# Kernel tuning notes

Measured on AMD Instinct MI355X. Metric: run time of the kernel, lower is better.

Reference implementation:

```python
import jax, jax.numpy as jnp
import numpy as np
from jax import lax

B = 128      # graphs per batch
N = 68       # facial landmarks (num_nodes per graph)
C = 3        # input channels
P = 32       # PATCH_SIZE
K = 16       # NUM_KERNELS
FD = 64      # feature_dim
GH = 128     # gcn_hidden_dim
OUT = 2      # output_dim
EG = 8 * N   # edges per graph
T = B * N    # total nodes


def setup_inputs() -> dict:
    key = jax.random.key(0)
    ks = jax.random.split(key, 8)
    x = jax.random.normal(ks[0], (T, C, P, P), jnp.float32)
    e = jax.random.randint(ks[1], (2, B, EG), 0, N)
    offs = (jnp.arange(B) * N)[None, :, None]
    edge_index = (e + offs).reshape(2, -1)            # within-graph edges, global ids
    batch = jnp.repeat(jnp.arange(B), N)              # node -> graph id
    conv_w = jax.random.normal(ks[2], (N, K, C, 3, 3), jnp.float32) * 0.05
    conv_b = jnp.zeros((N, K), jnp.float32)
    lin1_w = jax.random.normal(ks[3], (N, K * (P // 2) * (P // 2), FD), jnp.float32) * 0.02
    lin1_b = jnp.zeros((N, FD), jnp.float32)
    gcn_w = jax.random.normal(ks[4], (FD, GH), jnp.float32) * 0.1
    gcn_b = jnp.zeros((GH,), jnp.float32)
    mlp_w1 = jax.random.normal(ks[5], (GH, GH // 2), jnp.float32) * 0.1
    mlp_b1 = jnp.zeros((GH // 2,), jnp.float32)
    mlp_w2 = jax.random.normal(ks[6], (GH // 2, OUT), jnp.float32) * 0.1
    mlp_b2 = jnp.zeros((OUT,), jnp.float32)
    return dict(x=x, edge_index=edge_index, batch=batch, conv_w=conv_w, conv_b=conv_b,
                lin1_w=lin1_w, lin1_b=lin1_b, gcn_w=gcn_w, gcn_b=gcn_b,
                mlp_w1=mlp_w1, mlp_b1=mlp_b1, mlp_w2=mlp_w2, mlp_b2=mlp_b2)


def reference(x, edge_index, batch, conv_w, conv_b, lin1_w, lin1_b,
              gcn_w, gcn_b, mlp_w1, mlp_b1, mlp_w2, mlp_b2):
    # --- per-node-type CNN routing (nodes are laid out [graph, local_index]) ---
    xr = x.reshape(B, N, C, P, P)

    def cnn_one(xn, w, b):           # xn: [B,C,P,P]  w: [K,C,3,3]
        y = lax.conv_general_dilated(xn, w, (1, 1), 'SAME',
                                     dimension_numbers=('NCHW', 'OIHW', 'NCHW'))
        return jax.nn.relu(y + b[None, :, None, None])

    a = jax.vmap(cnn_one, in_axes=(1, 0, 0), out_axes=1)(xr, conv_w, conv_b)  # [B,N,K,P,P]
    pooled = lax.reduce_window(a, -jnp.inf, lax.max,
                               (1, 1, 1, 2, 2), (1, 1, 1, 2, 2), 'VALID')     # [B,N,K,P/2,P/2]
    flat = pooled.reshape(B, N, -1)
    feats = jax.nn.relu(jnp.einsum('bnf,nfo->bno', flat, lin1_w) + lin1_b[None])  # [B,N,FD]
    nodes = feats.reshape(T, FD)

    # --- GCNConv: add self-loops, symmetric normalization ---
    loop = jnp.arange(T)
    src = jnp.concatenate([edge_index[0], loop])
    dst = jnp.concatenate([edge_index[1], loop])
    deg = jax.ops.segment_sum(jnp.ones_like(dst, jnp.float32), dst, T)
    dis = jnp.where(deg > 0, 1.0 / jnp.sqrt(deg), 0.0)
    norm = dis[src] * dis[dst]
    xw = nodes @ gcn_w                                   # [T,GH]
    h = jax.ops.segment_sum(norm[:, None] * xw[src], dst, T) + gcn_b
    h = jax.nn.relu(h)

    # --- global mean pool over graphs ---
    cnt = jax.ops.segment_sum(jnp.ones((T,), jnp.float32), batch, B)
    g = jax.ops.segment_sum(h, batch, B) / cnt[:, None]  # [B,GH]

    # --- MLP head ---
    z = jax.nn.relu(g @ mlp_w1 + mlp_b1)
    return z @ mlp_w2 + mlp_b2                           # [B,OUT]
```

## Files before the change

### kernel.cpp

```cpp
#include <hip/hip_runtime.h>
#include <hip/hip_fp16.h>

#define B_   128
#define N_   68
#define C_   3
#define P_   32
#define K_   16
#define FD_  64
#define GH_  128
#define EG_  544
#define T_   8704
#define FLAT_ 4096
#define FCH_ 16

typedef __attribute__((ext_vector_type(8))) _Float16 half8;
typedef __attribute__((ext_vector_type(2))) _Float16 half2v;
typedef __attribute__((ext_vector_type(4))) float   floatx4;

__global__ __launch_bounds__(256) void conv_pool_kernel(
    const float* __restrict__ x, const float* __restrict__ conv_w,
    const float* __restrict__ conv_b, _Float16* __restrict__ pooled) {
  const int t = blockIdx.x;
  const int n = t % N_;
  const int tid = threadIdx.x;

  __shared__ float xs[3 * 34 * 34];
  __shared__ float wS[K_ * 28];

  {
    const float* wp = conv_w + (size_t)n * (K_ * 27);
    const float* bp = conv_b + (size_t)n * K_;
    for (int i = tid; i < K_ * 28; i += 256) {
      int k = i / 28, j = i - k * 28;
      wS[i] = (j < 27) ? wp[k * 27 + j] : bp[k];
    }
  }
  for (int i = tid; i < 396; i += 256) {
    int c = i / 132, j = i - c * 132;
    int off;
    if (j < 34)       off = j;
    else if (j < 68)  off = 33 * 34 + (j - 34);
    else if (j < 100) off = (j - 68 + 1) * 34;
    else              off = (j - 100 + 1) * 34 + 33;
    xs[c * 1156 + off] = 0.0f;
  }
  const float4* xg = (const float4*)(x + (size_t)t * (C_ * P_ * P_));
  #pragma unroll
  for (int j = 0; j < 3; j++) {
    int i4 = tid + j * 256;
    float4 v = xg[i4];
    int f0 = i4 * 4;
    int c = f0 >> 10, rem = f0 & 1023, y = rem >> 5, xc = rem & 31;
    float* dstp = &xs[c * 1156 + (y + 1) * 34 + xc + 1];
    dstp[0] = v.x; dstp[1] = v.y; dstp[2] = v.z; dstp[3] = v.w;
  }
  __syncthreads();

  const int py = tid >> 4, px = tid & 15;

  float xr[3][4][4];
  #pragma unroll
  for (int c = 0; c < 3; c++)
    #pragma unroll
    for (int r = 0; r < 4; r++)
      #pragma unroll
      for (int cc = 0; cc < 4; cc++)
        xr[c][r][cc] = xs[c * 1156 + (2 * py + r) * 34 + (2 * px + cc)];

  _Float16* outp = pooled + (size_t)t * FLAT_ + py * 16 + px;

  #pragma unroll 2
  for (int k = 0; k < K_; k++) {
    float w[28];
    const float4* wk4 = (const float4*)&wS[k * 28];
    #pragma unroll
    for (int q4 = 0; q4 < 7; q4++) *(float4*)&w[q4 * 4] = wk4[q4];
    float bk = w[27];
    float a00 = bk, a01 = bk, a10 = bk, a11 = bk;
    #pragma unroll
    for (int c = 0; c < 3; c++)
      #pragma unroll
      for (int dy = 0; dy < 3; dy++)
        #pragma unroll
        for (int dx = 0; dx < 3; dx++) {
          float wv = w[c * 9 + dy * 3 + dx];
          a00 += xr[c][dy][dx]         * wv;
          a01 += xr[c][dy][dx + 1]     * wv;
          a10 += xr[c][dy + 1][dx]     * wv;
          a11 += xr[c][dy + 1][dx + 1] * wv;
        }
    float m = fmaxf(fmaxf(a00, a01), fmaxf(a10, a11));
    m = fmaxf(m, 0.0f);
    outp[k * 256] = (_Float16)m;
  }
}

__global__ __launch_bounds__(256) void lin1_mfma_kernel(
    const _Float16* __restrict__ pooled, const float* __restrict__ lin1_w,
    float* __restrict__ part) {
  const int n   = blockIdx.x >> 4;
  const int fc  = blockIdx.x & 15;
  const int tid = threadIdx.x;
  const int wave = tid >> 6, lane = tid & 63;
  const int q = lane >> 4, lr = lane & 15;

  __shared__ __align__(16) _Float16 As[128 * 72];
  __shared__ __align__(16) _Float16 Bt[64 * 72];

  floatx4 acc[2][4];
  #pragma unroll
  for (int mt = 0; mt < 2; mt++)
    #pragma unroll
    for (int nt = 0; nt < 4; nt++)
      acc[mt][nt] = (floatx4){0.f, 0.f, 0.f, 0.f};

  const int f_base = fc * 256;
  for (int step = 0; step < 4; step++) {
    const int f0 = f_base + step * 64;

    #pragma unroll
    for (int j = 0; j < 4; j++) {
      int idx = tid + j * 256;
      int r = idx >> 3, ch = idx & 7;
      uint4 v = *(const uint4*)&pooled[(size_t)(r * N_ + n) * FLAT_ + f0 + ch * 8];
      *(uint4*)&As[r * 72 + ch * 8] = v;
    }
    const float* wg = &lin1_w[(size_t)n * (FLAT_ * FD_) + (size_t)f0 * FD_];
    #pragma unroll
    for (int it = 0; it < 2; it++) {
      int p = tid + it * 256;
      int o0 = (p & 15) * 4, k0 = (p >> 4) * 2;
      const float* wgk = wg + k0 * 64 + o0;
      float4 va = *(const float4*)wgk;
      float4 vb = *(const float4*)(wgk + 64);
      *(half2v*)&Bt[(o0 + 0) * 72 + k0] = (half2v){(_Float16)va.x, (_Float16)vb.x};
      *(half2v*)&Bt[(o0 + 1) * 72 + k0] = (half2v){(_Float16)va.y, (_Float16)vb.y};
      *(half2v*)&Bt[(o0 + 2) * 72 + k0] = (half2v){(_Float16)va.z, (_Float16)vb.z};
      *(half2v*)&Bt[(o0 + 3) * 72 + k0] = (half2v){(_Float16)va.w, (_Float16)vb.w};
    }
    __syncthreads();

    #pragma unroll
    for (int kh = 0; kh < 2; kh++) {
      half8 af[2], bf[4];
      #pragma unroll
      for (int mt = 0; mt < 2; mt++)
        af[mt] = *(const half8*)&As[(wave * 32 + mt * 16 + lr) * 72 + kh * 32 + q * 8];
      #pragma unroll
      for (int nt = 0; nt < 4; nt++)
        bf[nt] = *(const half8*)&Bt[(nt * 16 + lr) * 72 + kh * 32 + q * 8];
      #pragma unroll
      for (int mt = 0; mt < 2; mt++)
        #pragma unroll
        for (int nt = 0; nt < 4; nt++)
          acc[mt][nt] = __builtin_amdgcn_mfma_f32_16x16x32_f16(
              af[mt], bf[nt], acc[mt][nt], 0, 0, 0);
    }
    __syncthreads();
  }

  float* pb = part + (size_t)fc * T_ * FD_;
  #pragma unroll
  for (int mt = 0; mt < 2; mt++) {
    #pragma unroll
    for (int v = 0; v < 4; v++) {
      int r = wave * 32 + mt * 16 + q * 4 + v;
      size_t base = (size_t)(r * N_ + n) * FD_;
      #pragma unroll
      for (int nt = 0; nt < 4; nt++)
        pb[base + nt * 16 + lr] = acc[mt][nt][v];
    }
  }
}

__global__ __launch_bounds__(256) void feats_kernel(
    const float* __restrict__ part, const float* __restrict__ lin1_b,
    float* __restrict__ feats) {
  int gid = blockIdx.x * 256 + threadIdx.x;
  int t = gid >> 4, f4 = (gid & 15) * 4;
  int n = t % N_;
  float4 s = *(const float4*)&lin1_b[n * FD_ + f4];
  #pragma unroll
  for (int fc = 0; fc < FCH_; fc++) {
    float4 v = *(const float4*)&part[((size_t)fc * T_ + t) * FD_ + f4];
    s.x += v.x; s.y += v.y; s.z += v.z; s.w += v.w;
  }
  s.x = fmaxf(s.x, 0.f); s.y = fmaxf(s.y, 0.f);
  s.z = fmaxf(s.z, 0.f); s.w = fmaxf(s.w, 0.f);
  *(float4*)&feats[(size_t)t * FD_ + f4] = s;
}

__global__ __launch_bounds__(256) void gcn_agg_kernel(
    const float* __restrict__ feats, const int* __restrict__ edge_index,
    float* __restrict__ agg) {
  const int b  = blockIdx.x >> 1;
  const int fh = blockIdx.x & 1;
  const int tid = threadIdx.x;

  __shared__ float fS[N_ * 33], aS[N_ * 33];
  __shared__ int   esrcS[EG_], edstS[EG_];
  __shared__ float nrmS[EG_];
  __shared__ int   degS[N_];
  __shared__ float disS[N_];

  if (tid < N_) degS[tid] = 0;
  const int* srcp = edge_index;
  const int* dstp = edge_index + (B_ * EG_);
  const int e0 = b * EG_, nbase = b * N_;
  for (int e = tid; e < EG_; e += 256) {
    esrcS[e] = srcp[e0 + e] - nbase;
    edstS[e] = dstp[e0 + e] - nbase;
  }
  for (int idx = tid; idx < N_ * 32; idx += 256) {
    int i = idx >> 5, f = idx & 31;
    fS[i * 33 + f] = feats[(size_t)(b * N_ + i) * FD_ + fh * 32 + f];
  }
  __syncthreads();
  for (int e = tid; e < EG_; e += 256) atomicAdd(&degS[edstS[e]], 1);
  __syncthreads();
  if (tid < N_) disS[tid] = rsqrtf((float)(degS[tid] + 1));
  __syncthreads();
  for (int e = tid; e < EG_; e += 256)
    nrmS[e] = disS[esrcS[e]] * disS[edstS[e]];
  for (int idx = tid; idx < N_ * 32; idx += 256) {
    int i = idx >> 5, f = idx & 31;
    float d = disS[i];
    aS[i * 33 + f] = d * d * fS[i * 33 + f];
  }
  __syncthreads();
  for (int idx = tid; idx < EG_ * 32; idx += 256) {
    int e = idx >> 5, f = idx & 31;
    atomicAdd(&aS[edstS[e] * 33 + f], nrmS[e] * fS[esrcS[e] * 33 + f]);
  }
  __syncthreads();
  for (int idx = tid; idx < N_ * 32; idx += 256) {
    int i = idx >> 5, f = idx & 31;
    agg[(size_t)(b * N_ + i) * FD_ + fh * 32 + f] = aS[i * 33 + f];
  }
}

__global__ __launch_bounds__(512) void gcn_head_kernel(
    const float* __restrict__ agg, const float* __restrict__ gcn_w,
    const float* __restrict__ gcn_b, const float* __restrict__ w1,
    const float* __restrict__ b1, const float* __restrict__ w2,
    const float* __restrict__ b2, float* __restrict__ out) {
  const int b = blockIdx.x;
  const int tid = threadIdx.x;

  __shared__ float aS[N_ * 68];
  __shared__ float wS[FD_ * GH_];
  __shared__ float gP[4][GH_];
  __shared__ float z1S[64];

  for (int i4 = tid; i4 < N_ * 16; i4 += 512) {
    int i = i4 >> 4, qf = (i4 & 15) * 4;
    *(float4*)&aS[i * 68 + qf] = *(const float4*)&agg[(size_t)(b * N_ + i) * FD_ + qf];
  }
  #pragma unroll
  for (int j = 0; j < 4; j++)
    ((float4*)wS)[tid + j * 512] = ((const float4*)gcn_w)[tid + j * 512];
  __syncthreads();

  const int j = tid & 127, ig = tid >> 7;
  float wc[64];
  #pragma unroll
  for (int k = 0; k < 64; k++) wc[k] = wS[k * GH_ + j];
  const float bias = gcn_b[j];
  float gsum = 0.f;
  for (int i = ig; i < N_; i += 4) {
    float acc = bias;
    #pragma unroll
    for (int kq = 0; kq < 16; kq++) {
      float4 a = *(const float4*)&aS[i * 68 + kq * 4];
      acc += a.x * wc[kq * 4] + a.y * wc[kq * 4 + 1]
           + a.z * wc[kq * 4 + 2] + a.w * wc[kq * 4 + 3];
    }
    gsum += fmaxf(acc, 0.f);
  }
  gP[ig][j] = gsum;
  __syncthreads();
  if (tid < GH_)
    gP[0][tid] = (gP[0][tid] + gP[1][tid] + gP[2][tid] + gP[3][tid]) * (1.f / 68.f);
  __syncthreads();
  if (tid < 64) {
    float s = b1[tid];
    #pragma unroll 8
    for (int jj = 0; jj < GH_; jj++) s += gP[0][jj] * w1[jj * 64 + tid];
    z1S[tid] = fmaxf(s, 0.f);
  }
  __syncthreads();
  if (tid < 2) {
    float s = b2[tid];
    #pragma unroll 8
    for (int jj = 0; jj < 64; jj++) s += z1S[jj] * w2[jj * 2 + tid];
    out[b * 2 + tid] = s;
  }
}

extern "C" void kernel_launch(void* const* d_in, const int* in_sizes, int n_in,
                              void* d_out, int out_size, void* d_ws, size_t ws_size,
                              hipStream_t stream) {
  const float* x        = (const float*)d_in[0];
  const int*   edge_idx = (const int*)d_in[1];
  const float* conv_w   = (const float*)d_in[3];
  const float* conv_b   = (const float*)d_in[4];
  const float* lin1_w   = (const float*)d_in[5];
  const float* lin1_b   = (const float*)d_in[6];
  const float* gcn_w    = (const float*)d_in[7];
  const float* gcn_b    = (const float*)d_in[8];
  const float* mlp_w1   = (const float*)d_in[9];
  const float* mlp_b1   = (const float*)d_in[10];
  const float* mlp_w2   = (const float*)d_in[11];
  const float* mlp_b2   = (const float*)d_in[12];
  float* outp = (float*)d_out;

  char* wsb = (char*)d_ws;
  _Float16* pooled = (_Float16*)wsb;
  float* part  = (float*)(wsb + (size_t)T_ * FLAT_ * 2);
  float* feats = part + (size_t)FCH_ * T_ * FD_;
  float* agg   = feats + (size_t)T_ * FD_;

  conv_pool_kernel<<<T_, 256, 0, stream>>>(x, conv_w, conv_b, pooled);
  lin1_mfma_kernel<<<N_ * FCH_, 256, 0, stream>>>(pooled, lin1_w, part);
  feats_kernel<<<544, 256, 0, stream>>>(part, lin1_b, feats);
  gcn_agg_kernel<<<B_ * 2, 256, 0, stream>>>(feats, edge_idx, agg);
  gcn_head_kernel<<<B_, 512, 0, stream>>>(agg, gcn_w, gcn_b,
                                          mlp_w1, mlp_b1, mlp_w2, mlp_b2, outp);
}
```

Baseline: 355.7 us.

## Fuse GCN tail kernels, prefetch lin1 tiles, pack conv FMAs into float2

Merges feats reduction, GCN aggregation and head into one kernel per graph, which removes two launches and the feats/agg round trips through global memory. lin1 now prefetches the next A/B tile into registers while the MFMAs on the current tile run. The conv kernel packs row pairs into float2 vectors so the compiler can emit packed FMAs, and it adds an occupancy hint to its launch bounds. The fused tail uses fewer blocks (128 instead of 256 for aggregation) and more LDS per block, so parallelism in that stage drops.

```diff
diff --git a/kernel.cpp b/kernel.cpp
--- a/kernel.cpp
+++ b/kernel.cpp
@@ -16,8 +16,9 @@
 typedef __attribute__((ext_vector_type(8))) _Float16 half8;
 typedef __attribute__((ext_vector_type(2))) _Float16 half2v;
 typedef __attribute__((ext_vector_type(4))) float   floatx4;
-
-__global__ __launch_bounds__(256) void conv_pool_kernel(
+typedef __attribute__((ext_vector_type(2))) float   v2f;
+
+__global__ __launch_bounds__(256, 3) void conv_pool_kernel(
     const float* __restrict__ x, const float* __restrict__ conv_w,
     const float* __restrict__ conv_b, _Float16* __restrict__ pooled) {
   const int t = blockIdx.x;
@@ -67,6 +68,15 @@
       for (int cc = 0; cc < 4; cc++)
         xr[c][r][cc] = xs[c * 1156 + (2 * py + r) * 34 + (2 * px + cc)];
 
+  v2f vp[3][3][4];
+  #pragma unroll
+  for (int c = 0; c < 3; c++)
+    #pragma unroll
+    for (int rp = 0; rp < 3; rp++)
+      #pragma unroll
+      for (int col = 0; col < 4; col++)
+        vp[c][rp][col] = (v2f){xr[c][rp][col], xr[c][rp + 1][col]};
+
   _Float16* outp = pooled + (size_t)t * FLAT_ + py * 16 + px;
 
   #pragma unroll 2
@@ -76,20 +86,20 @@
     #pragma unroll
     for (int q4 = 0; q4 < 7; q4++) *(float4*)&w[q4 * 4] = wk4[q4];
     float bk = w[27];
-    float a00 = bk, a01 = bk, a10 = bk, a11 = bk;
+    v2f a0 = {bk, bk};
+    v2f a1 = {bk, bk};
     #pragma unroll
     for (int c = 0; c < 3; c++)
       #pragma unroll
       for (int dy = 0; dy < 3; dy++)
         #pragma unroll
         for (int dx = 0; dx < 3; dx++) {
-          float wv = w[c * 9 + dy * 3 + dx];
-          a00 += xr[c][dy][dx]         * wv;
-          a01 += xr[c][dy][dx + 1]     * wv;
-          a10 += xr[c][dy + 1][dx]     * wv;
-          a11 += xr[c][dy + 1][dx + 1] * wv;
+          float wsc = w[c * 9 + dy * 3 + dx];
+          v2f wv = {wsc, wsc};
+          a0 += vp[c][dy][dx]     * wv;
+          a1 += vp[c][dy][dx + 1] * wv;
         }
-    float m = fmaxf(fmaxf(a00, a01), fmaxf(a10, a11));
+    float m = fmaxf(fmaxf(a0.x, a0.y), fmaxf(a1.x, a1.y));
     m = fmaxf(m, 0.0f);
     outp[k * 256] = (_Float16)m;
   }
@@ -115,30 +125,66 @@
       acc[mt][nt] = (floatx4){0.f, 0.f, 0.f, 0.f};
 
   const int f_base = fc * 256;
-  for (int step = 0; step < 4; step++) {
-    const int f0 = f_base + step * 64;
-
+  const float* wbase = lin1_w + (size_t)n * (FLAT_ * FD_);
+
+  uint4  aR[4];
+  float4 bR[4];
+  {
+    const int f0 = f_base;
     #pragma unroll
     for (int j = 0; j < 4; j++) {
       int idx = tid + j * 256;
       int r = idx >> 3, ch = idx & 7;
-      uint4 v = *(const uint4*)&pooled[(size_t)(r * N_ + n) * FLAT_ + f0 + ch * 8];
-      *(uint4*)&As[r * 72 + ch * 8] = v;
-    }
-    const float* wg = &lin1_w[(size_t)n * (FLAT_ * FD_) + (size_t)f0 * FD_];
+      aR[j] = *(const uint4*)&pooled[(size_t)(r * N_ + n) * FLAT_ + f0 + ch * 8];
+    }
+    const float* wg = wbase + (size_t)f0 * FD_;
     #pragma unroll
     for (int it = 0; it < 2; it++) {
       int p = tid + it * 256;
       int o0 = (p & 15) * 4, k0 = (p >> 4) * 2;
       const float* wgk = wg + k0 * 64 + o0;
-      float4 va = *(const float4*)wgk;
-      float4 vb = *(const float4*)(wgk + 64);
+      bR[it * 2]     = *(const float4*)wgk;
+      bR[it * 2 + 1] = *(const float4*)(wgk + 64);
+    }
+  }
+
+  for (int step = 0; step < 4; step++) {
+    #pragma unroll
+    for (int j = 0; j < 4; j++) {
+      int idx = tid + j * 256;
+      int r = idx >> 3, ch = idx & 7;
+      *(uint4*)&As[r * 72 + ch * 8] = aR[j];
+    }
+    #pragma unroll
+    for (int it = 0; it < 2; it++) {
+      int p = tid + it * 256;
+      int o0 = (p & 15) * 4, k0 = (p >> 4) * 2;
+      float4 va = bR[it * 2], vb = bR[it * 2 + 1];
       *(half2v*)&Bt[(o0 + 0) * 72 + k0] = (half2v){(_Float16)va.x, (_Float16)vb.x};
       *(half2v*)&Bt[(o0 + 1) * 72 + k0] = (half2v){(_Float16)va.y, (_Float16)vb.y};
       *(half2v*)&Bt[(o0 + 2) * 72 + k0] = (half2v){(_Float16)va.z, (_Float16)vb.z};
       *(half2v*)&Bt[(o0 + 3) * 72 + k0] = (half2v){(_Float16)va.w, (_Float16)vb.w};
     }
     __syncthreads();
+
+    if (step < 3) {
+      const int f0 = f_base + (step + 1) * 64;
+      #pragma unroll
+      for (int j = 0; j < 4; j++) {
+        int idx = tid + j * 256;
+        int r = idx >> 3, ch = idx & 7;
+        aR[j] = *(const uint4*)&pooled[(size_t)(r * N_ + n) * FLAT_ + f0 + ch * 8];
+      }
+      const float* wg = wbase + (size_t)f0 * FD_;
+      #pragma unroll
+      for (int it = 0; it < 2; it++) {
+        int p = tid + it * 256;
+        int o0 = (p & 15) * 4, k0 = (p >> 4) * 2;
+        const float* wgk = wg + k0 * 64 + o0;
+        bR[it * 2]     = *(const float4*)wgk;
+        bR[it * 2 + 1] = *(const float4*)(wgk + 64);
+      }
+    }
 
     #pragma unroll
     for (int kh = 0; kh < 2; kh++) {
@@ -173,92 +219,70 @@
   }
 }
 
-__global__ __launch_bounds__(256) void feats_kernel(
-    const float* __restrict__ part, const float* __restrict__ lin1_b,
-    float* __restrict__ feats) {
-  int gid = blockIdx.x * 256 + threadIdx.x;
-  int t = gid >> 4, f4 = (gid & 15) * 4;
-  int n = t % N_;
-  float4 s = *(const float4*)&lin1_b[n * FD_ + f4];
-  #pragma unroll
-  for (int fc = 0; fc < FCH_; fc++) {
-    float4 v = *(const float4*)&part[((size_t)fc * T_ + t) * FD_ + f4];
-    s.x += v.x; s.y += v.y; s.z += v.z; s.w += v.w;
-  }
-  s.x = fmaxf(s.x, 0.f); s.y = fmaxf(s.y, 0.f);
-  s.z = fmaxf(s.z, 0.f); s.w = fmaxf(s.w, 0.f);
-  *(float4*)&feats[(size_t)t * FD_ + f4] = s;
-}
-
-__global__ __launch_bounds__(256) void gcn_agg_kernel(
-    const float* __restrict__ feats, const int* __restrict__ edge_index,
-    float* __restrict__ agg) {
-  const int b  = blockIdx.x >> 1;
-  const int fh = blockIdx.x & 1;
-  const int tid = threadIdx.x;
-
-  __shared__ float fS[N_ * 33], aS[N_ * 33];
-  __shared__ int   esrcS[EG_], edstS[EG_];
-  __shared__ float nrmS[EG_];
-  __shared__ int   degS[N_];
-  __shared__ float disS[N_];
-
-  if (tid < N_) degS[tid] = 0;
-  const int* srcp = edge_index;
-  const int* dstp = edge_index + (B_ * EG_);
-  const int e0 = b * EG_, nbase = b * N_;
-  for (int e = tid; e < EG_; e += 256) {
-    esrcS[e] = srcp[e0 + e] - nbase;
-    edstS[e] = dstp[e0 + e] - nbase;
-  }
-  for (int idx = tid; idx < N_ * 32; idx += 256) {
-    int i = idx >> 5, f = idx & 31;
-    fS[i * 33 + f] = feats[(size_t)(b * N_ + i) * FD_ + fh * 32 + f];
-  }
-  __syncthreads();
-  for (int e = tid; e < EG_; e += 256) atomicAdd(&degS[edstS[e]], 1);
-  __syncthreads();
-  if (tid < N_) disS[tid] = rsqrtf((float)(degS[tid] + 1));
-  __syncthreads();
-  for (int e = tid; e < EG_; e += 256)
-    nrmS[e] = disS[esrcS[e]] * disS[edstS[e]];
-  for (int idx = tid; idx < N_ * 32; idx += 256) {
-    int i = idx >> 5, f = idx & 31;
-    float d = disS[i];
-    aS[i * 33 + f] = d * d * fS[i * 33 + f];
-  }
-  __syncthreads();
-  for (int idx = tid; idx < EG_ * 32; idx += 256) {
-    int e = idx >> 5, f = idx & 31;
-    atomicAdd(&aS[edstS[e] * 33 + f], nrmS[e] * fS[esrcS[e] * 33 + f]);
-  }
-  __syncthreads();
-  for (int idx = tid; idx < N_ * 32; idx += 256) {
-    int i = idx >> 5, f = idx & 31;
-    agg[(size_t)(b * N_ + i) * FD_ + fh * 32 + f] = aS[i * 33 + f];
-  }
-}
-
-__global__ __launch_bounds__(512) void gcn_head_kernel(
-    const float* __restrict__ agg, const float* __restrict__ gcn_w,
+__global__ __launch_bounds__(512) void tail_kernel(
+    const float* __restrict__ part, const int* __restrict__ edge_index,
+    const float* __restrict__ lin1_b, const float* __restrict__ gcn_w,
     const float* __restrict__ gcn_b, const float* __restrict__ w1,
     const float* __restrict__ b1, const float* __restrict__ w2,
     const float* __restrict__ b2, float* __restrict__ out) {
   const int b = blockIdx.x;
   const int tid = threadIdx.x;
 
+  __shared__ float fS[N_ * 68];
   __shared__ float aS[N_ * 68];
   __shared__ float wS[FD_ * GH_];
+  __shared__ int   esrcS[EG_], edstS[EG_];
+  __shared__ float nrmS[EG_];
+  __shared__ int   degS[N_];
+  __shared__ float disS[N_];
   __shared__ float gP[4][GH_];
   __shared__ float z1S[64];
 
-  for (int i4 = tid; i4 < N_ * 16; i4 += 512) {
-    int i = i4 >> 4, qf = (i4 & 15) * 4;
-    *(float4*)&aS[i * 68 + qf] = *(const float4*)&agg[(size_t)(b * N_ + i) * FD_ + qf];
+  if (tid < N_) degS[tid] = 0;
+  const int* srcp = edge_index;
+  const int* dstp = edge_index + (B_ * EG_);
+  const int e0 = b * EG_, nbase = b * N_;
+  for (int e = tid; e < EG_; e += 512) {
+    esrcS[e] = srcp[e0 + e] - nbase;
+    edstS[e] = dstp[e0 + e] - nbase;
+  }
+  for (int idx4 = tid; idx4 < N_ * 16; idx4 += 512) {
+    int i  = idx4 >> 4;
+    int f4 = (idx4 & 15) * 4;
+    int t  = b * N_ + i;
+    float4 s = *(const float4*)&lin1_b[i * FD_ + f4];
+    #pragma unroll
+    for (int fc = 0; fc < FCH_; fc++) {
+      float4 v = *(const float4*)&part[((size_t)fc * T_ + t) * FD_ + f4];
+      s.x += v.x; s.y += v.y; s.z += v.z; s.w += v.w;
+    }
+    s.x = fmaxf(s.x, 0.f); s.y = fmaxf(s.y, 0.f);
+    s.z = fmaxf(s.z, 0.f); s.w = fmaxf(s.w, 0.f);
+    *(float4*)&fS[i * 68 + f4] = s;
   }
   #pragma unroll
   for (int j = 0; j < 4; j++)
     ((float4*)wS)[tid + j * 512] = ((const float4*)gcn_w)[tid + j * 512];
+  __syncthreads();
+
+  for (int e = tid; e < EG_; e += 512) atomicAdd(&degS[edstS[e]], 1);
+  __syncthreads();
+  if (tid < N_) disS[tid] = rsqrtf((float)(degS[tid] + 1));
+  __syncthreads();
+  for (int e = tid; e < EG_; e += 512)
+    nrmS[e] = disS[esrcS[e]] * disS[edstS[e]];
+  for (int idx4 = tid; idx4 < N_ * 16; idx4 += 512) {
+    int i = idx4 >> 4, f4 = (idx4 & 15) * 4;
+    float d2 = disS[i] * disS[i];
+    float4 v = *(const float4*)&fS[i * 68 + f4];
+    v.x *= d2; v.y *= d2; v.z *= d2; v.w *= d2;
+    *(float4*)&aS[i * 68 + f4] = v;
+  }
+  __syncthreads();
+  for (int idx = tid; idx < EG_ * FD_; idx += 512) {
+    int e = idx >> 6, f = idx & 63;
+    atomicAdd(&aS[edstS[e] * 68 + f], nrmS[e] * fS[esrcS[e] * 68 + f]);
+  }
   __syncthreads();
 
   const int j = tid & 127, ig = tid >> 7;
@@ -317,13 +341,9 @@
   char* wsb = (char*)d_ws;
   _Float16* pooled = (_Float16*)wsb;
   float* part  = (float*)(wsb + (size_t)T_ * FLAT_ * 2);
-  float* feats = part + (size_t)FCH_ * T_ * FD_;
-  float* agg   = feats + (size_t)T_ * FD_;
 
   conv_pool_kernel<<<T_, 256, 0, stream>>>(x, conv_w, conv_b, pooled);
   lin1_mfma_kernel<<<N_ * FCH_, 256, 0, stream>>>(pooled, lin1_w, part);
-  feats_kernel<<<544, 256, 0, stream>>>(part, lin1_b, feats);
-  gcn_agg_kernel<<<B_ * 2, 256, 0, stream>>>(feats, edge_idx, agg);
-  gcn_head_kernel<<<B_, 512, 0, stream>>>(agg, gcn_w, gcn_b,
-                                          mlp_w1, mlp_b1, mlp_w2, mlp_b2, outp);
+  tail_kernel<<<B_, 512, 0, stream>>>(part, edge_idx, lin1_b, gcn_w, gcn_b,
+                                      mlp_w1, mlp_b1, mlp_w2, mlp_b2, outp);
 }
```

New measurement: 375.6 us. 5.6% more time.
